# Kernel tuning notes

Measured on AMD Instinct MI355X. Metric: run time of the kernel, lower is better.

Reference implementation:

```python
import jax, jax.numpy as jnp
import numpy as np

HID = 1024
HEADS = 16
HEAD_DIM = HID // HEADS
MAX_P = 64
TAB = 2 * MAX_P + 1
B, L = 8, 512


def setup_inputs() -> dict:
    key = jax.random.key(0)
    ks = jax.random.split(key, 16)
    def lin(k, fan_in, fan_out):
        lim = 1.0 / np.sqrt(fan_in)
        kw, kb = jax.random.split(k)
        W = jax.random.uniform(kw, (fan_out, fan_in), jnp.float32, -lim, lim)
        b = jax.random.uniform(kb, (fan_out,), jnp.float32, -lim, lim)
        return W, b
    Wq, bq = lin(ks[0], HID, HID)
    Wk, bk = lin(ks[1], HID, HID)
    Wv, bv = lin(ks[2], HID, HID)
    Wo, bo = lin(ks[3], HID, HID)
    # xavier_uniform for relative-position tables
    xlim = float(np.sqrt(6.0 / (TAB + HEAD_DIM)))
    table_k = jax.random.uniform(ks[4], (TAB, HEAD_DIM), jnp.float32, -xlim, xlim)
    table_v = jax.random.uniform(ks[5], (TAB, HEAD_DIM), jnp.float32, -xlim, xlim)
    return {
        "query": jax.random.normal(ks[6], (B, L, HID), jnp.float32),
        "key": jax.random.normal(ks[7], (B, L, HID), jnp.float32),
        "value": jax.random.normal(ks[8], (B, L, HID), jnp.float32),
        "final_mat": jax.random.randint(ks[9], (B, L, L), 0, TAB, jnp.int64 if jax.config.jax_enable_x64 else jnp.int32),
        "Wq": Wq, "bq": bq, "Wk": Wk, "bk": bk,
        "Wv": Wv, "bv": bv, "Wo": Wo, "bo": bo,
        "table_k": table_k, "table_v": table_v,
    }


def reference(query, key, value, final_mat, Wq, bq, Wk, bk, Wv, bv, Wo, bo, table_k, table_v):
    Bt, Lq, D = query.shape
    H, hd = HEADS, HEAD_DIM
    q = query @ Wq.T + bq          # [B,Lq,D]
    k = key @ Wk.T + bk            # [B,Lk,D]
    v = value @ Wv.T + bv          # [B,Lv,D]
    q4 = q.reshape(Bt, Lq, H, hd)
    k4 = k.reshape(Bt, -1, H, hd)
    v4 = v.reshape(Bt, -1, H, hd)
    # content-content scores
    attn1 = jnp.einsum('bqhd,bkhd->bhqk', q4, k4)
    # content-position scores via gathered relative-key embeddings [B,Lq,Lk,hd]
    rk = table_k[final_mat]
    attn2 = jnp.einsum('bqhd,bqkd->bhqk', q4, rk)
    scale = jnp.asarray(np.sqrt(hd), q.dtype)
    attn = jax.nn.softmax((attn1 + attn2) / scale, axis=-1)  # [B,H,Lq,Lk]
    # dropout p=0 (eval)
    w1 = jnp.einsum('bhqk,bkhd->bqhd', attn, v4)
    rv = table_v[final_mat]                                   # [B,Lq,Lk,hd]
    w2 = jnp.einsum('bhqk,bqkd->bqhd', attn, rv)
    x = (w1 + w2).reshape(Bt, Lq, D)
    return x @ Wo.T + bo
```

## Files before the change

kernel.cpp:

```cpp
#include <hip/hip_runtime.h>

#define HID 1024
#define HEADS 16
#define HD 64
#define TAB 129
#define QSTR 136
#define BATCH 8
#define SEQ 512

typedef unsigned int uint;
typedef unsigned short ushort;
typedef __attribute__((ext_vector_type(4))) float f32x4;
typedef __attribute__((ext_vector_type(8))) __bf16 bf16x8;

__device__ __forceinline__ ushort f2b(float x) {
    uint b = __float_as_uint(x);
    uint r = (b + 0x7fffu + ((b >> 16) & 1u)) >> 16;
    return (ushort)r;
}
__device__ __forceinline__ uint pk(float lo, float hi) {
    return (uint)f2b(lo) | ((uint)f2b(hi) << 16);
}
__device__ __forceinline__ float b2f(ushort u) {
    return __uint_as_float(((uint)u) << 16);
}
union U16x8 { uint u[4]; bf16x8 v; ushort s[8]; uint4 q; };
__device__ __forceinline__ bf16x8 pack8(float a0, float a1, float a2, float a3,
                                        float a4, float a5, float a6, float a7) {
    U16x8 r;
    r.u[0] = pk(a0, a1); r.u[1] = pk(a2, a3);
    r.u[2] = pk(a4, a5); r.u[3] = pk(a6, a7);
    return r.v;
}

#define GL16(gp, lp) __builtin_amdgcn_global_load_lds( \
    (const __attribute__((address_space(1))) void*)(gp), \
    (__attribute__((address_space(3))) void*)(lp), 16, 0, 0)

#define LDS_BARRIER() do { \
        asm volatile("s_waitcnt lgkmcnt(0)" ::: "memory"); \
        __builtin_amdgcn_s_barrier(); \
    } while (0)

struct ConvArgs { const float* src[7]; ushort* dst[7]; };

__global__ __launch_bounds__(256) void convert_bf16(ConvArgs ca) {
    int bid = blockIdx.x;
    int ti, lb;
    if (bid < 6144) { ti = bid >> 11; lb = bid & 2047; }
    else { int r = bid - 6144; ti = 3 + (r >> 9); lb = r & 511; }
    const float* s = ca.src[ti] + (size_t)lb * 2048 + (threadIdx.x << 3);
    ushort*      d = ca.dst[ti] + (size_t)lb * 2048 + (threadIdx.x << 3);
    float4 a = *(const float4*)s;
    float4 c = *(const float4*)(s + 4);
    uint4 u;
    u.x = pk(a.x, a.y); u.y = pk(a.z, a.w);
    u.z = pk(c.x, c.y); u.w = pk(c.z, c.w);
    *(uint4*)d = u;
}

struct GemmArgs {
    const ushort* A[3];
    const ushort* W[3];
    const float*  bias[3];
    float*        Cf[3];
    ushort*       Cb[3];
};

__global__ __launch_bounds__(256) void gemm_bf16(GemmArgs ga, int M, int N, int K) {
    __shared__ ushort As[2][128 * 32];
    __shared__ ushort Bs[2][128 * 32];
    const int z = blockIdx.z;
    const ushort* A = ga.A[z];
    const ushort* W = ga.W[z];
    const int tid = threadIdx.x;
    const int m0 = blockIdx.y * 128;
    const int n0 = blockIdx.x * 128;

    const int w  = tid >> 6;
    const int l  = tid & 63;
    const int lr = l & 15;
    const int lg = l >> 4;
    const int wm = w >> 1;
    const int wn = w & 1;

    const int sr = tid >> 2;
    const int sc = tid & 3;
    const int g  = sc ^ ((sr >> 1) & 3);
    const ushort* Ag0 = A + (size_t)(m0 + sr)      * K + g * 8;
    const ushort* Ag1 = A + (size_t)(m0 + sr + 64) * K + g * 8;
    const ushort* Wg0 = W + (size_t)(n0 + sr)      * K + g * 8;
    const ushort* Wg1 = W + (size_t)(n0 + sr + 64) * K + g * 8;

    f32x4 acc[4][4];
#pragma unroll
    for (int mt = 0; mt < 4; ++mt)
#pragma unroll
        for (int nt = 0; nt < 4; ++nt) acc[mt][nt] = (f32x4){0.f, 0.f, 0.f, 0.f};

#define STAGE(buf, k0) do { \
        GL16(Ag0 + (k0), &As[buf][w * 512]); \
        GL16(Ag1 + (k0), &As[buf][2048 + w * 512]); \
        GL16(Wg0 + (k0), &Bs[buf][w * 512]); \
        GL16(Wg1 + (k0), &Bs[buf][2048 + w * 512]); \
    } while (0)

    const int swz = (lr >> 1) & 3;
#define COMPUTE(buf) do { \
        bf16x8 af[4], bf[4]; \
        _Pragma("unroll") \
        for (int mt = 0; mt < 4; ++mt) \
            af[mt] = *(const bf16x8*)&As[buf][(wm * 64 + mt * 16 + lr) * 32 + (lg ^ swz) * 8]; \
        _Pragma("unroll") \
        for (int nt = 0; nt < 4; ++nt) \
            bf[nt] = *(const bf16x8*)&Bs[buf][(wn * 64 + nt * 16 + lr) * 32 + (lg ^ swz) * 8]; \
        _Pragma("unroll") \
        for (int mt = 0; mt < 4; ++mt) \
            _Pragma("unroll") \
            for (int nt = 0; nt < 4; ++nt) \
                acc[mt][nt] = __builtin_amdgcn_mfma_f32_16x16x32_bf16(af[mt], bf[nt], acc[mt][nt], 0, 0, 0); \
    } while (0)

    STAGE(0, 0);
    __syncthreads();
    const int nk = K / 32;
    for (int t = 0; t < nk - 1; ++t) {
        STAGE((t + 1) & 1, (size_t)(t + 1) * 32);
        COMPUTE(t & 1);
        __syncthreads();
    }
    COMPUTE((nk - 1) & 1);

    const float* bias = ga.bias[z];
    float bv[4];
#pragma unroll
    for (int nt = 0; nt < 4; ++nt) bv[nt] = bias[n0 + wn * 64 + nt * 16 + lr];
    float*  Cf = ga.Cf[z];
    ushort* Cb = ga.Cb[z];
    if (Cf) {
#pragma unroll
        for (int mt = 0; mt < 4; ++mt)
#pragma unroll
            for (int r4 = 0; r4 < 4; ++r4) {
                size_t m = m0 + wm * 64 + mt * 16 + lg * 4 + r4;
                float* crow = Cf + m * N + n0 + wn * 64 + lr;
#pragma unroll
                for (int nt = 0; nt < 4; ++nt)
                    crow[nt * 16] = acc[mt][nt][r4] + bv[nt];
            }
    } else {
#pragma unroll
        for (int mt = 0; mt < 4; ++mt)
#pragma unroll
            for (int r4 = 0; r4 < 4; ++r4) {
                size_t m = m0 + wm * 64 + mt * 16 + lg * 4 + r4;
                ushort* crow = Cb + m * N + n0 + wn * 64 + lr;
#pragma unroll
                for (int nt = 0; nt < 4; ++nt)
                    crow[nt * 16] = f2b(acc[mt][nt][r4] + bv[nt]);
            }
    }
#undef STAGE
#undef COMPUTE
}

__global__ __launch_bounds__(256) void gemm_wo(const ushort* __restrict__ A,
                                               const ushort* __restrict__ W,
                                               const float* __restrict__ bias,
                                               float* __restrict__ Cf) {
    const int M = BATCH * SEQ, N = HID, K = HID;
    __shared__ ushort As[2][128 * 32];
    __shared__ ushort Bs[2][64 * 32];
    const int tid = threadIdx.x;
    const int m0 = blockIdx.y * 128;
    const int n0 = blockIdx.x * 64;

    const int w  = tid >> 6;
    const int l  = tid & 63;
    const int lr = l & 15;
    const int lg = l >> 4;
    const int wm = w >> 1;
    const int wn = w & 1;

    const int sr = tid >> 2;
    const int sc = tid & 3;
    const int g  = sc ^ ((sr >> 1) & 3);
    const ushort* Ag0 = A + (size_t)(m0 + sr)      * K + g * 8;
    const ushort* Ag1 = A + (size_t)(m0 + sr + 64) * K + g * 8;
    const ushort* Wg0 = W + (size_t)(n0 + sr)      * K + g * 8;

    f32x4 acc[4][2];
#pragma unroll
    for (int mt = 0; mt < 4; ++mt)
#pragma unroll
        for (int nt = 0; nt < 2; ++nt) acc[mt][nt] = (f32x4){0.f, 0.f, 0.f, 0.f};

#define STAGE(buf, k0) do { \
        GL16(Ag0 + (k0), &As[buf][w * 512]); \
        GL16(Ag1 + (k0), &As[buf][2048 + w * 512]); \
        GL16(Wg0 + (k0), &Bs[buf][w * 512]); \
    } while (0)

    const int swz = (lr >> 1) & 3;
#define COMPUTE(buf) do { \
        bf16x8 af[4], bf[2]; \
        _Pragma("unroll") \
        for (int mt = 0; mt < 4; ++mt) \
            af[mt] = *(const bf16x8*)&As[buf][(wm * 64 + mt * 16 + lr) * 32 + (lg ^ swz) * 8]; \
        _Pragma("unroll") \
        for (int nt = 0; nt < 2; ++nt) \
            bf[nt] = *(const bf16x8*)&Bs[buf][(wn * 32 + nt * 16 + lr) * 32 + (lg ^ swz) * 8]; \
        _Pragma("unroll") \
        for (int mt = 0; mt < 4; ++mt) \
            _Pragma("unroll") \
            for (int nt = 0; nt < 2; ++nt) \
                acc[mt][nt] = __builtin_amdgcn_mfma_f32_16x16x32_bf16(af[mt], bf[nt], acc[mt][nt], 0, 0, 0); \
    } while (0)

    STAGE(0, 0);
    __syncthreads();
    const int nk = K / 32;
    for (int t = 0; t < nk - 1; ++t) {
        STAGE((t + 1) & 1, (size_t)(t + 1) * 32);
        COMPUTE(t & 1);
        __syncthreads();
    }
    COMPUTE((nk - 1) & 1);

    float bv[2];
#pragma unroll
    for (int nt = 0; nt < 2; ++nt) bv[nt] = bias[n0 + wn * 32 + nt * 16 + lr];
#pragma unroll
    for (int mt = 0; mt < 4; ++mt)
#pragma unroll
        for (int r4 = 0; r4 < 4; ++r4) {
            size_t m = m0 + wm * 64 + mt * 16 + lg * 4 + r4;
            float* crow = Cf + m * N + n0 + wn * 32 + lr;
#pragma unroll
            for (int nt = 0; nt < 2; ++nt)
                crow[nt * 16] = acc[mt][nt][r4] + bv[nt];
        }
#undef STAGE
#undef COMPUTE
}

__global__ __launch_bounds__(256) void prep_kernel(const ushort* __restrict__ qb,
                                                   const float* __restrict__ table_k,
                                                   const ushort* __restrict__ vb,
                                                   const float* __restrict__ table_v,
                                                   ushort* __restrict__ qtab,
                                                   ushort* __restrict__ vT,
                                                   ushort* __restrict__ tvT) {
    __shared__ __align__(16) ushort shmem[144 * 72];
    const int wg  = blockIdx.x;
    const int tid = threadIdx.x;

    if (wg < 256) {
        const int h    = wg & 15;
        const int half = (wg >> 4) & 1;
        const int b    = wg >> 5;
        const int q0   = half * 256;
        ushort* tk = shmem;
        for (int i = tid; i < TAB * 8; i += 256) {
            int row = i >> 3, gr = i & 7;
            const float* src = table_k + row * HD + gr * 8;
            float4 a = *(const float4*)src;
            float4 c = *(const float4*)(src + 4);
            uint4 u;
            u.x = pk(a.x, a.y); u.y = pk(a.z, a.w);
            u.z = pk(c.x, c.y); u.w = pk(c.z, c.w);
            *(uint4*)&tk[row * 72 + gr * 8] = u;
        }
        __syncthreads();

        const int w  = tid >> 6;
        const int l  = tid & 63;
        const int lr = l & 15;
        const int lg = l >> 4;
        bf16x8 qf[4][2];
#pragma unroll
        for (int qt = 0; qt < 4; ++qt) {
            const ushort* qrow = qb + ((size_t)(b * SEQ) + q0 + w * 64 + qt * 16 + lr) * HID + h * HD;
            qf[qt][0] = *(const bf16x8*)(qrow + lg * 8);
            qf[qt][1] = *(const bf16x8*)(qrow + 32 + lg * 8);
        }
        ushort* outbase = qtab + ((size_t)(b * HEADS + h) * SEQ + q0 + w * 64) * QSTR;
#pragma unroll
        for (int mt = 0; mt < 9; ++mt) {
            bf16x8 tf0 = *(const bf16x8*)&tk[(mt * 16 + lr) * 72 + lg * 8];
            bf16x8 tf1 = *(const bf16x8*)&tk[(mt * 16 + lr) * 72 + 32 + lg * 8];
#pragma unroll
            for (int qt = 0; qt < 4; ++qt) {
                f32x4 acc = (f32x4){0.f, 0.f, 0.f, 0.f};
                acc = __builtin_amdgcn_mfma_f32_16x16x32_bf16(tf0, qf[qt][0], acc, 0, 0, 0);
                acc = __builtin_amdgcn_mfma_f32_16x16x32_bf16(tf1, qf[qt][1], acc, 0, 0, 0);
                ushort* orow = outbase + (size_t)(qt * 16 + lr) * QSTR;
                if (mt < 8) {
                    uint2 pu;
                    pu.x = pk(acc[0], acc[1]); pu.y = pk(acc[2], acc[3]);
                    *(uint2*)&orow[mt * 16 + lg * 4] = pu;
                } else if (lg == 0) {
                    orow[128] = f2b(acc[0]);
                }
            }
        }
    } else if (wg < 768) {
        const int vw = wg - 256;
        ushort* tile = shmem;
        const int b = vw >> 6, h = (vw >> 2) & 15, kc = vw & 3;
        const int k0 = kc * 128;
        {
            const int kr = tid >> 1, dc = (tid & 1) * 32;
            const ushort* src = vb + ((size_t)(b * SEQ) + k0 + kr) * HID + h * 64 + dc;
#pragma unroll
            for (int j = 0; j < 4; ++j) {
                uint4 u = *(const uint4*)(src + j * 8);
                *(uint4*)&tile[kr * 72 + dc + j * 8] = u;
            }
        }
        __syncthreads();
        {
            const int dr = tid >> 2, kc2 = (tid & 3) * 32;
            ushort* dst = vT + ((size_t)(b * 16 + h) * 64 + dr) * 512 + k0 + kc2;
#pragma unroll
            for (int j = 0; j < 4; ++j) {
                U16x8 o;
#pragma unroll
                for (int i = 0; i < 8; ++i)
                    o.s[i] = tile[(kc2 + j * 8 + i) * 72 + dr];
                *(uint4*)(dst + j * 8) = o.q;
            }
        }
    } else {
        const int tt = tid >> 1, dc = (tid & 1) * 32;
        const float* src = table_v + (size_t)tt * HD + dc;
#pragma unroll
        for (int i = 0; i < 32; ++i)
            tvT[(size_t)(dc + i) * 128 + tt] = f2b(src[i]);
    }
}

__global__ __launch_bounds__(256, 3) void attn_mfma(const ushort* __restrict__ qp,
                                                    const ushort* __restrict__ kp,
                                                    const ushort* __restrict__ vT,
                                                    const ushort* __restrict__ qt,
                                                    const int* __restrict__ fmat,
                                                    const float* __restrict__ table_v,
                                                    const ushort* __restrict__ tvT,
                                                    ushort* __restrict__ x) {
    constexpr float FIX = 65536.0f;
    constexpr float INV_FIX = 1.0f / 65536.0f;

    __shared__ __align__(16) ushort qtb[16 * QSTR];
    __shared__ __align__(16) uint   sbin[16 * 132];
    __shared__ __align__(16) ushort P[4][16 * 136];
    __shared__ float rowsumw[4][16];

    const int tid = threadIdx.x;
    const int w   = tid >> 6;
    const int l   = tid & 63;
    const int lr  = l & 15;
    const int lg  = l >> 4;

    const int wg   = blockIdx.x;
    const int work = (wg & 7) * 512 + (wg >> 3);
    const int qblk = work & 31;
    const int h    = (work >> 5) & 15;
    const int b    = work >> 9;
    const int q0   = qblk * 16;
    const size_t bSEQ = (size_t)b * SEQ;
    const int hHD = h * HD;

    const int*    fmrow    = fmat + (bSEQ + q0 + lr) * SEQ;
    const ushort* kfr_base = kp + (bSEQ + lr) * HID + hHD;
    const ushort* vfr_base = vT + ((size_t)(b * HEADS + h) * HD + lr) * SEQ;

    bf16x8 qfrag[2];
    {
        const ushort* qrow = qp + (bSEQ + q0 + lr) * HID + hHD;
        qfrag[0] = *(const bf16x8*)(qrow + lg * 8);
        qfrag[1] = *(const bf16x8*)(qrow + 32 + lg * 8);
    }

    {
        const uint4* src = (const uint4*)(qt + ((size_t)(b * HEADS + h) * SEQ + q0) * QSTR);
        uint4* dst = (uint4*)qtb;
        for (int i = tid; i < 16 * QSTR / 8; i += 256) dst[i] = src[i];
    }
    {
        uint4 z = {0u, 0u, 0u, 0u};
        uint4* dz = (uint4*)sbin;
        for (int i = tid; i < 16 * 132 / 4; i += 256) dz[i] = z;
    }
    LDS_BARRIER();

    f32x4 stv[8];
    int4  fmr[8];
#pragma unroll
    for (int i = 0; i < 8; ++i) {
        const int t  = i >> 2;
        const int mt = i & 3;
        const int k0 = (w * 2 + t) * 64;
        const ushort* kr = kfr_base + (size_t)(k0 + mt * 16) * HID;
        bf16x8 ka0 = *(const bf16x8*)(kr + lg * 8);
        bf16x8 ka1 = *(const bf16x8*)(kr + 32 + lg * 8);
        fmr[i] = *(const int4*)&fmrow[k0 + mt * 16 + lg * 4];
        f32x4 st = (f32x4){0.f, 0.f, 0.f, 0.f};
        st = __builtin_amdgcn_mfma_f32_16x16x32_bf16(ka0, qfrag[0], st, 0, 0, 0);
        st = __builtin_amdgcn_mfma_f32_16x16x32_bf16(ka1, qfrag[1], st, 0, 0, 0);
        stv[i] = st;
    }

    float lsum = 0.f;
#pragma unroll
    for (int i = 0; i < 8; ++i) {
        const int t  = i >> 2;
        const int mt = i & 3;
        const int4 fm4 = fmr[i];
        const f32x4 st = stv[i];
        float pr0 = __expf((st[0] + b2f(qtb[lr * QSTR + fm4.x])) * 0.125f);
        float pr1 = __expf((st[1] + b2f(qtb[lr * QSTR + fm4.y])) * 0.125f);
        float pr2 = __expf((st[2] + b2f(qtb[lr * QSTR + fm4.z])) * 0.125f);
        float pr3 = __expf((st[3] + b2f(qtb[lr * QSTR + fm4.w])) * 0.125f);
        lsum += pr0 + pr1 + pr2 + pr3;
        __hip_atomic_fetch_add(&sbin[lr * 132 + fm4.x], (uint)(pr0 * FIX),
                               __ATOMIC_RELAXED, __HIP_MEMORY_SCOPE_WORKGROUP);
        __hip_atomic_fetch_add(&sbin[lr * 132 + fm4.y], (uint)(pr1 * FIX),
                               __ATOMIC_RELAXED, __HIP_MEMORY_SCOPE_WORKGROUP);
        __hip_atomic_fetch_add(&sbin[lr * 132 + fm4.z], (uint)(pr2 * FIX),
                               __ATOMIC_RELAXED, __HIP_MEMORY_SCOPE_WORKGROUP);
        __hip_atomic_fetch_add(&sbin[lr * 132 + fm4.w], (uint)(pr3 * FIX),
                               __ATOMIC_RELAXED, __HIP_MEMORY_SCOPE_WORKGROUP);
        uint2 pu;
        pu.x = pk(pr0, pr1); pu.y = pk(pr2, pr3);
        *(uint2*)&P[w][lr * 136 + t * 64 + mt * 16 + lg * 4] = pu;
    }
    lsum += __shfl_xor(lsum, 16);
    lsum += __shfl_xor(lsum, 32);
    if (lg == 0) rowsumw[w][lr] = lsum;

    f32x4 acc_o[4];
#pragma unroll
    for (int nt = 0; nt < 4; ++nt) acc_o[nt] = (f32x4){0.f, 0.f, 0.f, 0.f};
#pragma unroll
    for (int t = 0; t < 2; ++t) {
        const int k0 = (w * 2 + t) * 64;
        bf16x8 pa0 = *(const bf16x8*)&P[w][lr * 136 + t * 64 + lg * 8];
        bf16x8 pa1 = *(const bf16x8*)&P[w][lr * 136 + t * 64 + 32 + lg * 8];
#pragma unroll
        for (int nt = 0; nt < 4; ++nt) {
            const ushort* vr = vfr_base + (size_t)nt * 16 * SEQ + k0;
            bf16x8 vb0 = *(const bf16x8*)(vr + lg * 8);
            bf16x8 vb1 = *(const bf16x8*)(vr + 32 + lg * 8);
            acc_o[nt] = __builtin_amdgcn_mfma_f32_16x16x32_bf16(pa0, vb0, acc_o[nt], 0, 0, 0);
            acc_o[nt] = __builtin_amdgcn_mfma_f32_16x16x32_bf16(pa1, vb1, acc_o[nt], 0, 0, 0);
        }
    }

    LDS_BARRIER();

    {
        const uint* sp = &sbin[lr * 132 + w * 32 + lg * 8];
        bf16x8 af = pack8((float)sp[0] * INV_FIX, (float)sp[1] * INV_FIX,
                          (float)sp[2] * INV_FIX, (float)sp[3] * INV_FIX,
                          (float)sp[4] * INV_FIX, (float)sp[5] * INV_FIX,
                          (float)sp[6] * INV_FIX, (float)sp[7] * INV_FIX);
#pragma unroll
        for (int nt = 0; nt < 4; ++nt) {
            bf16x8 bf_ = *(const bf16x8*)(tvT + (size_t)(nt * 16 + lr) * 128 + w * 32 + lg * 8);
            acc_o[nt] = __builtin_amdgcn_mfma_f32_16x16x32_bf16(af, bf_, acc_o[nt], 0, 0, 0);
        }
    }

    float* obuf = (float*)&P[0][0];
    if (w != 0) {
#pragma unroll
        for (int nt = 0; nt < 4; ++nt)
            *(f32x4*)&obuf[(((w - 1) * 4 + nt) * 64 + l) * 4] = acc_o[nt];
    }
    LDS_BARRIER();

    if (w == 0) {
#pragma unroll
        for (int j = 0; j < 3; ++j)
#pragma unroll
            for (int nt = 0; nt < 4; ++nt) {
                f32x4 p_ = *(const f32x4*)&obuf[((j * 4 + nt) * 64 + l) * 4];
                acc_o[nt][0] += p_[0]; acc_o[nt][1] += p_[1];
                acc_o[nt][2] += p_[2]; acc_o[nt][3] += p_[3];
            }
        float iv[4], nb[4];
#pragma unroll
        for (int r = 0; r < 4; ++r) {
            const int q = lg * 4 + r;
            iv[r] = 1.f / (rowsumw[0][q] + rowsumw[1][q] + rowsumw[2][q] + rowsumw[3][q]);
            nb[r] = (float)sbin[q * 132 + 128] * INV_FIX;
        }
        ushort* orow = x + (bSEQ + q0 + lg * 4) * HID + hHD;
#pragma unroll
        for (int nt = 0; nt < 4; ++nt) {
            float tv = table_v[(size_t)128 * HD + nt * 16 + lr];
#pragma unroll
            for (int r = 0; r < 4; ++r) {
                float o = (acc_o[nt][r] + nb[r] * tv) * iv[r];
                orow[(size_t)r * HID + nt * 16 + lr] = f2b(o);
            }
        }
    }
}

extern "C" void kernel_launch(void* const* d_in, const int* in_sizes, int n_in,
                              void* d_out, int out_size, void* d_ws, size_t ws_size,
                              hipStream_t stream) {
    const float* query = (const float*)d_in[0];
    const float* key   = (const float*)d_in[1];
    const float* value = (const float*)d_in[2];
    const int*   fmat  = (const int*)d_in[3];
    const float* Wq = (const float*)d_in[4];
    const float* bq = (const float*)d_in[5];
    const float* Wk = (const float*)d_in[6];
    const float* bk = (const float*)d_in[7];
    const float* Wv = (const float*)d_in[8];
    const float* bv = (const float*)d_in[9];
    const float* Wo = (const float*)d_in[10];
    const float* bo = (const float*)d_in[11];
    const float* table_k = (const float*)d_in[12];
    const float* table_v = (const float*)d_in[13];

    const size_t nBLD = (size_t)BATCH * SEQ * HID;
    const size_t nW   = (size_t)HID * HID;
    ushort* us = (ushort*)d_ws;
    ushort* qin16 = us;                 us += nBLD;
    ushort* kin16 = us;                 us += nBLD;
    ushort* vin16 = us;                 us += nBLD;
    ushort* wq16  = us;                 us += nW;
    ushort* wk16  = us;                 us += nW;
    ushort* wv16  = us;                 us += nW;
    ushort* wo16  = us;                 us += nW;
    ushort* qb16  = us;                 us += nBLD;
    ushort* kb16  = us;                 us += nBLD;
    ushort* vb16  = us;                 us += nBLD;
    ushort* qt16  = us;                 us += (size_t)BATCH * HEADS * SEQ * QSTR;
    ushort* xb16  = us;                 us += nBLD;

    ConvArgs ca;
    ca.src[0] = query; ca.src[1] = key; ca.src[2] = value;
    ca.src[3] = Wq; ca.src[4] = Wk; ca.src[5] = Wv; ca.src[6] = Wo;
    ca.dst[0] = qin16; ca.dst[1] = kin16; ca.dst[2] = vin16;
    ca.dst[3] = wq16; ca.dst[4] = wk16; ca.dst[5] = wv16; ca.dst[6] = wo16;
    convert_bf16<<<dim3(8192), 256, 0, stream>>>(ca);

    const int M = BATCH * SEQ;

    GemmArgs gq = {};
    gq.A[0] = qin16; gq.A[1] = kin16; gq.A[2] = vin16;
    gq.W[0] = wq16;  gq.W[1] = wk16;  gq.W[2] = wv16;
    gq.bias[0] = bq; gq.bias[1] = bk; gq.bias[2] = bv;
    gq.Cf[0] = nullptr; gq.Cf[1] = nullptr; gq.Cf[2] = nullptr;
    gq.Cb[0] = qb16; gq.Cb[1] = kb16; gq.Cb[2] = vb16;
    gemm_bf16<<<dim3(HID / 128, M / 128, 3), 256, 0, stream>>>(gq, M, HID, HID);

    ushort* vTbuf  = qin16;
    ushort* tvTbuf = kin16;

    prep_kernel<<<dim3(769), 256, 0, stream>>>(qb16, table_k, vb16, table_v,
                                               qt16, vTbuf, tvTbuf);

    attn_mfma<<<dim3(BATCH * HEADS * (SEQ/16)), 256, 0, stream>>>(
        qb16, kb16, vTbuf, qt16, fmat, table_v, tvTbuf, xb16);

    gemm_wo<<<dim3(HID / 64, M / 128), 256, 0, stream>>>(xb16, wo16, bo, (float*)d_out);
}
```

Measured before the change: 192.0 us.

## Compress final_mat to uint8 in prep and batch attention fragment loads

Adds 1024 blocks to the prep kernel that pack the int32 relative-position indices into a uint8 copy, so each of the 16 head-blocks reading the same rows in attention fetches a quarter of the bytes. The attention kernel also issues all K and V fragment loads up front, pinned in registers with empty asm barriers, before the MFMAs to expose more memory-level parallelism. The trade-offs are an extra read/write pass over final_mat in prep and higher register pressure under the 3-waves launch bound. The byte packing relies on indices being below 256.

```diff
diff --git a/kernel.cpp b/kernel.cpp
--- a/kernel.cpp
+++ b/kernel.cpp
@@ -10,6 +10,7 @@
 
 typedef unsigned int uint;
 typedef unsigned short ushort;
+typedef unsigned char uchar;
 typedef __attribute__((ext_vector_type(4))) float f32x4;
 typedef __attribute__((ext_vector_type(8))) __bf16 bf16x8;
 
@@ -31,6 +32,14 @@
     r.u[0] = pk(a0, a1); r.u[1] = pk(a2, a3);
     r.u[2] = pk(a4, a5); r.u[3] = pk(a6, a7);
     return r.v;
+}
+
+__device__ __forceinline__ void keep(bf16x8& v) {
+    uint4* u = (uint4*)&v;
+    asm volatile("" : "+v"(u->x), "+v"(u->y), "+v"(u->z), "+v"(u->w));
+}
+__device__ __forceinline__ void keepu(uint& v) {
+    asm volatile("" : "+v"(v));
 }
 
 #define GL16(gp, lp) __builtin_amdgcn_global_load_lds( \
@@ -248,9 +257,11 @@
                                                    const float* __restrict__ table_k,
                                                    const ushort* __restrict__ vb,
                                                    const float* __restrict__ table_v,
+                                                   const int* __restrict__ fmat,
                                                    ushort* __restrict__ qtab,
                                                    ushort* __restrict__ vT,
-                                                   ushort* __restrict__ tvT) {
+                                                   ushort* __restrict__ tvT,
+                                                   uchar* __restrict__ fm8) {
     __shared__ __align__(16) ushort shmem[144 * 72];
     const int wg  = blockIdx.x;
     const int tid = threadIdx.x;
@@ -331,12 +342,20 @@
                 *(uint4*)(dst + j * 8) = o.q;
             }
         }
-    } else {
+    } else if (wg == 768) {
         const int tt = tid >> 1, dc = (tid & 1) * 32;
         const float* src = table_v + (size_t)tt * HD + dc;
 #pragma unroll
         for (int i = 0; i < 32; ++i)
             tvT[(size_t)(dc + i) * 128 + tt] = f2b(src[i]);
+    } else {
+        const size_t base = (size_t)(wg - 769) * 2048 + (size_t)tid * 8;
+        int4 a = *(const int4*)(fmat + base);
+        int4 c = *(const int4*)(fmat + base + 4);
+        uint lo = (uint)a.x | ((uint)a.y << 8) | ((uint)a.z << 16) | ((uint)a.w << 24);
+        uint hi = (uint)c.x | ((uint)c.y << 8) | ((uint)c.z << 16) | ((uint)c.w << 24);
+        uint2 o; o.x = lo; o.y = hi;
+        *(uint2*)(fm8 + base) = o;
     }
 }
 
@@ -344,7 +363,7 @@
                                                     const ushort* __restrict__ kp,
                                                     const ushort* __restrict__ vT,
                                                     const ushort* __restrict__ qt,
-                                                    const int* __restrict__ fmat,
+                                                    const uchar* __restrict__ fm8,
                                                     const float* __restrict__ table_v,
                                                     const ushort* __restrict__ tvT,
                                                     ushort* __restrict__ x) {
@@ -371,7 +390,7 @@
     const size_t bSEQ = (size_t)b * SEQ;
     const int hHD = h * HD;
 
-    const int*    fmrow    = fmat + (bSEQ + q0 + lr) * SEQ;
+    const uchar*  fmrow8   = fm8 + (bSEQ + q0 + lr) * SEQ;
     const ushort* kfr_base = kp + (bSEQ + lr) * HID + hHD;
     const ushort* vfr_base = vT + ((size_t)(b * HEADS + h) * HD + lr) * SEQ;
 
@@ -394,20 +413,27 @@
     }
     LDS_BARRIER();
 
-    f32x4 stv[8];
-    int4  fmr[8];
+    bf16x8 kfr[8][2];
+    uint   fmu[8];
 #pragma unroll
     for (int i = 0; i < 8; ++i) {
         const int t  = i >> 2;
         const int mt = i & 3;
         const int k0 = (w * 2 + t) * 64;
         const ushort* kr = kfr_base + (size_t)(k0 + mt * 16) * HID;
-        bf16x8 ka0 = *(const bf16x8*)(kr + lg * 8);
-        bf16x8 ka1 = *(const bf16x8*)(kr + 32 + lg * 8);
-        fmr[i] = *(const int4*)&fmrow[k0 + mt * 16 + lg * 4];
+        kfr[i][0] = *(const bf16x8*)(kr + lg * 8);
+        kfr[i][1] = *(const bf16x8*)(kr + 32 + lg * 8);
+        fmu[i] = *(const uint*)(fmrow8 + k0 + mt * 16 + lg * 4);
+    }
+#pragma unroll
+    for (int i = 0; i < 8; ++i) { keep(kfr[i][0]); keep(kfr[i][1]); keepu(fmu[i]); }
+
+    f32x4 stv[8];
+#pragma unroll
+    for (int i = 0; i < 8; ++i) {
         f32x4 st = (f32x4){0.f, 0.f, 0.f, 0.f};
-        st = __builtin_amdgcn_mfma_f32_16x16x32_bf16(ka0, qfrag[0], st, 0, 0, 0);
-        st = __builtin_amdgcn_mfma_f32_16x16x32_bf16(ka1, qfrag[1], st, 0, 0, 0);
+        st = __builtin_amdgcn_mfma_f32_16x16x32_bf16(kfr[i][0], qfrag[0], st, 0, 0, 0);
+        st = __builtin_amdgcn_mfma_f32_16x16x32_bf16(kfr[i][1], qfrag[1], st, 0, 0, 0);
         stv[i] = st;
     }
 
@@ -416,20 +442,21 @@
     for (int i = 0; i < 8; ++i) {
         const int t  = i >> 2;
         const int mt = i & 3;
-        const int4 fm4 = fmr[i];
+        const uint fm = fmu[i];
+        const int t0 = fm & 255, t1 = (fm >> 8) & 255, t2 = (fm >> 16) & 255, t3 = fm >> 24;
         const f32x4 st = stv[i];
-        float pr0 = __expf((st[0] + b2f(qtb[lr * QSTR + fm4.x])) * 0.125f);
-        float pr1 = __expf((st[1] + b2f(qtb[lr * QSTR + fm4.y])) * 0.125f);
-        float pr2 = __expf((st[2] + b2f(qtb[lr * QSTR + fm4.z])) * 0.125f);
-        float pr3 = __expf((st[3] + b2f(qtb[lr * QSTR + fm4.w])) * 0.125f);
+        float pr0 = __expf((st[0] + b2f(qtb[lr * QSTR + t0])) * 0.125f);
+        float pr1 = __expf((st[1] + b2f(qtb[lr * QSTR + t1])) * 0.125f);
+        float pr2 = __expf((st[2] + b2f(qtb[lr * QSTR + t2])) * 0.125f);
+        float pr3 = __expf((st[3] + b2f(qtb[lr * QSTR + t3])) * 0.125f);
         lsum += pr0 + pr1 + pr2 + pr3;
-        __hip_atomic_fetch_add(&sbin[lr * 132 + fm4.x], (uint)(pr0 * FIX),
+        __hip_atomic_fetch_add(&sbin[lr * 132 + t0], (uint)(pr0 * FIX),
                                __ATOMIC_RELAXED, __HIP_MEMORY_SCOPE_WORKGROUP);
-        __hip_atomic_fetch_add(&sbin[lr * 132 + fm4.y], (uint)(pr1 * FIX),
+        __hip_atomic_fetch_add(&sbin[lr * 132 + t1], (uint)(pr1 * FIX),
                                __ATOMIC_RELAXED, __HIP_MEMORY_SCOPE_WORKGROUP);
-        __hip_atomic_fetch_add(&sbin[lr * 132 + fm4.z], (uint)(pr2 * FIX),
+        __hip_atomic_fetch_add(&sbin[lr * 132 + t2], (uint)(pr2 * FIX),
                                __ATOMIC_RELAXED, __HIP_MEMORY_SCOPE_WORKGROUP);
-        __hip_atomic_fetch_add(&sbin[lr * 132 + fm4.w], (uint)(pr3 * FIX),
+        __hip_atomic_fetch_add(&sbin[lr * 132 + t3], (uint)(pr3 * FIX),
                                __ATOMIC_RELAXED, __HIP_MEMORY_SCOPE_WORKGROUP);
         uint2 pu;
         pu.x = pk(pr0, pr1); pu.y = pk(pr2, pr3);
@@ -439,21 +466,33 @@
     lsum += __shfl_xor(lsum, 32);
     if (lg == 0) rowsumw[w][lr] = lsum;
 
-    f32x4 acc_o[4];
-#pragma unroll
-    for (int nt = 0; nt < 4; ++nt) acc_o[nt] = (f32x4){0.f, 0.f, 0.f, 0.f};
+    bf16x8 vfr[2][4][2];
 #pragma unroll
     for (int t = 0; t < 2; ++t) {
         const int k0 = (w * 2 + t) * 64;
+#pragma unroll
+        for (int nt = 0; nt < 4; ++nt) {
+            const ushort* vr = vfr_base + (size_t)nt * 16 * SEQ + k0;
+            vfr[t][nt][0] = *(const bf16x8*)(vr + lg * 8);
+            vfr[t][nt][1] = *(const bf16x8*)(vr + 32 + lg * 8);
+        }
+    }
+#pragma unroll
+    for (int t = 0; t < 2; ++t)
+#pragma unroll
+        for (int nt = 0; nt < 4; ++nt) { keep(vfr[t][nt][0]); keep(vfr[t][nt][1]); }
+
+    f32x4 acc_o[4];
+#pragma unroll
+    for (int nt = 0; nt < 4; ++nt) acc_o[nt] = (f32x4){0.f, 0.f, 0.f, 0.f};
+#pragma unroll
+    for (int t = 0; t < 2; ++t) {
         bf16x8 pa0 = *(const bf16x8*)&P[w][lr * 136 + t * 64 + lg * 8];
         bf16x8 pa1 = *(const bf16x8*)&P[w][lr * 136 + t * 64 + 32 + lg * 8];
 #pragma unroll
         for (int nt = 0; nt < 4; ++nt) {
-            const ushort* vr = vfr_base + (size_t)nt * 16 * SEQ + k0;
-            bf16x8 vb0 = *(const bf16x8*)(vr + lg * 8);
-            bf16x8 vb1 = *(const bf16x8*)(vr + 32 + lg * 8);
-            acc_o[nt] = __builtin_amdgcn_mfma_f32_16x16x32_bf16(pa0, vb0, acc_o[nt], 0, 0, 0);
-            acc_o[nt] = __builtin_amdgcn_mfma_f32_16x16x32_bf16(pa1, vb1, acc_o[nt], 0, 0, 0);
+            acc_o[nt] = __builtin_amdgcn_mfma_f32_16x16x32_bf16(pa0, vfr[t][nt][0], acc_o[nt], 0, 0, 0);
+            acc_o[nt] = __builtin_amdgcn_mfma_f32_16x16x32_bf16(pa1, vfr[t][nt][1], acc_o[nt], 0, 0, 0);
         }
     }
 
@@ -542,6 +581,7 @@
     ushort* vb16  = us;                 us += nBLD;
     ushort* qt16  = us;                 us += (size_t)BATCH * HEADS * SEQ * QSTR;
     ushort* xb16  = us;                 us += nBLD;
+    uchar*  fm8   = (uchar*)us;
 
     ConvArgs ca;
     ca.src[0] = query; ca.src[1] = key; ca.src[2] = value;
@@ -563,11 +603,11 @@
     ushort* vTbuf  = qin16;
     ushort* tvTbuf = kin16;
 
-    prep_kernel<<<dim3(769), 256, 0, stream>>>(qb16, table_k, vb16, table_v,
-                                               qt16, vTbuf, tvTbuf);
+    prep_kernel<<<dim3(1793), 256, 0, stream>>>(qb16, table_k, vb16, table_v,
+                                                fmat, qt16, vTbuf, tvTbuf, fm8);
 
     attn_mfma<<<dim3(BATCH * HEADS * (SEQ/16)), 256, 0, stream>>>(
-        qb16, kb16, vTbuf, qt16, fmat, table_v, tvTbuf, xb16);
+        qb16, kb16, vTbuf, qt16, fm8, table_v, tvTbuf, xb16);
 
     gemm_wo<<<dim3(HID / 64, M / 128), 256, 0, stream>>>(xb16, wo16, bo, (float*)d_out);
 }
```

After: 198.6 us. 3.5% more time.
